# Kernel optimization log

Hardware: AMD Instinct MI355X
Metric: run time of the kernel (lower is better)

Reference implementation:

```python
import jax, jax.numpy as jnp
import numpy as np

B, N, C = 4, 8192, 512
H, Dh, G, R = 8, 64, 64, 2  # heads, dim_head, slice_num, mlp_ratio
EPS_LN = 1e-5
EPS_NORM = 1e-5


def _ln(x, g, b):
    m = jnp.mean(x, axis=-1, keepdims=True)
    v = jnp.var(x, axis=-1, keepdims=True)
    return (x - m) * jax.lax.rsqrt(v + EPS_LN) * g + b


def setup_inputs() -> dict:
    key = jax.random.key(0)
    ks = jax.random.split(key, 16)
    r = lambda k, shp: jax.random.normal(k, shp, jnp.float32) * 0.02
    inner = H * Dh
    return {
        "fx": jax.random.normal(ks[0], (B, N, C), jnp.float32),
        "ln1_g": jnp.ones((C,), jnp.float32), "ln1_b": jnp.zeros((C,), jnp.float32),
        "Wx": r(ks[1], (C, inner)), "bx": jnp.zeros((inner,), jnp.float32),
        "Wfx": r(ks[2], (C, inner)), "bfx": jnp.zeros((inner,), jnp.float32),
        "Wslice": r(ks[3], (Dh, G)), "bslice": jnp.zeros((G,), jnp.float32),
        "temperature": jnp.full((1, H, 1, 1), 0.5, jnp.float32),
        "Wq": r(ks[4], (Dh, Dh)), "Wk": r(ks[5], (Dh, Dh)), "Wv": r(ks[6], (Dh, Dh)),
        "Wout": r(ks[7], (inner, C)), "bout": jnp.zeros((C,), jnp.float32),
        "tln_g": jnp.ones((Dh,), jnp.float32), "tln_b": jnp.zeros((Dh,), jnp.float32),
        "Wm1": r(ks[8], (Dh, R * Dh)), "bm1": jnp.zeros((R * Dh,), jnp.float32),
        "Wm2": r(ks[9], (R * Dh, Dh)), "bm2": jnp.zeros((Dh,), jnp.float32),
    }


def reference(fx, ln1_g, ln1_b, Wx, bx, Wfx, bfx, Wslice, bslice, temperature,
              Wq, Wk, Wv, Wout, bout, tln_g, tln_b, Wm1, bm1, Wm2, bm2):
    fx_norm = _ln(fx, ln1_g, ln1_b)                          # [B,N,C]
    # _forward_slice: project to per-head mid features
    x_mid = (fx_norm @ Wx + bx).reshape(B, N, H, Dh).transpose(0, 2, 1, 3)   # [B,H,N,Dh]
    fx_mid = (fx_norm @ Wfx + bfx).reshape(B, N, H, Dh).transpose(0, 2, 1, 3)
    # _project_token: soft slice assignment + weighted pooling into G tokens
    logits = jnp.einsum('bhnd,dg->bhng', x_mid, Wslice) + bslice
    slice_w = jax.nn.softmax(logits / temperature, axis=-1)  # [B,H,N,G]
    slice_norm = jnp.sum(slice_w, axis=2)                    # [B,H,G]
    slice_tok = jnp.einsum('bhnd,bhng->bhgd', fx_mid, slice_w) / (slice_norm[..., None] + EPS_NORM)
    # attention over the small token set (G tokens)
    q = slice_tok @ Wq
    k = slice_tok @ Wk
    v = slice_tok @ Wv
    scale = Dh ** -0.5
    attn = jax.nn.softmax(jnp.einsum('bhgd,bhpd->bhgp', q, k) * scale, axis=-1)
    out_tok = jnp.einsum('bhgp,bhpd->bhgd', attn, v) + slice_tok
    # token MLP with residual
    h = _ln(out_tok, tln_g, tln_b)
    h = jax.nn.gelu(h @ Wm1 + bm1, approximate=False) @ Wm2 + bm2
    tokens = h + out_tok                                     # [B,H,G,Dh]
    # _deslice: weighted scatter back to N points, merge heads, out projection
    out_x = jnp.einsum('bhgd,bhng->bhnd', tokens, slice_w)
    out_x = out_x.transpose(0, 2, 1, 3).reshape(B, N, H * Dh)
    out = out_x @ Wout + bout
    return out + fx_norm
```

## Files before the change

kernel.cpp:

```cpp
#include <hip/hip_runtime.h>
#include <math.h>

#define B_ 4
#define N_ 8192
#define C_ 512
#define H_ 8
#define M_ (B_ * N_)

typedef __attribute__((ext_vector_type(8))) short bf16x8;
typedef __attribute__((ext_vector_type(4))) float f32x4;
typedef __attribute__((ext_vector_type(8))) unsigned short u16x8;
typedef __attribute__((ext_vector_type(4))) unsigned short u16x4;

__device__ __forceinline__ float b2f(unsigned short u) {
  union { unsigned int i; float f; } v;
  v.i = ((unsigned int)u) << 16;
  return v.f;
}
__device__ __forceinline__ unsigned short f2b(float f) {
  union { float f; unsigned int i; } v;
  v.f = f;
  unsigned int r = v.i + 0x7fff + ((v.i >> 16) & 1);
  return (unsigned short)(r >> 16);
}
__device__ __forceinline__ void gl_lds16(const void* g, void* l) {
  __builtin_amdgcn_global_load_lds(
      (const __attribute__((address_space(1))) unsigned int*)g,
      (__attribute__((address_space(3))) unsigned int*)l, 16, 0, 0);
}

__global__ __launch_bounds__(256) void ln_bf16(
    const float* __restrict__ x, const float* __restrict__ gam,
    const float* __restrict__ bet, unsigned short* __restrict__ y) {
  int wave = threadIdx.x >> 6, lane = threadIdx.x & 63;
  int row = (blockIdx.x << 2) + wave;
  const float4* xr = (const float4*)(x + (size_t)row * C_);
  float4 v0 = xr[lane], v1 = xr[lane + 64];
  float s = v0.x + v0.y + v0.z + v0.w + v1.x + v1.y + v1.z + v1.w;
  float q = v0.x * v0.x + v0.y * v0.y + v0.z * v0.z + v0.w * v0.w +
            v1.x * v1.x + v1.y * v1.y + v1.z * v1.z + v1.w * v1.w;
#pragma unroll
  for (int off = 32; off; off >>= 1) {
    s += __shfl_xor(s, off);
    q += __shfl_xor(q, off);
  }
  float mean = s * (1.0f / C_);
  float var = q * (1.0f / C_) - mean * mean;
  float rstd = rsqrtf(var + 1e-5f);
  const float4* gr = (const float4*)gam;
  const float4* br = (const float4*)bet;
  float4 g0 = gr[lane], g1 = gr[lane + 64];
  float4 b0 = br[lane], b1 = br[lane + 64];
  u16x4 oa, ob;
  oa.x = f2b((v0.x - mean) * rstd * g0.x + b0.x);
  oa.y = f2b((v0.y - mean) * rstd * g0.y + b0.y);
  oa.z = f2b((v0.z - mean) * rstd * g0.z + b0.z);
  oa.w = f2b((v0.w - mean) * rstd * g0.w + b0.w);
  ob.x = f2b((v1.x - mean) * rstd * g1.x + b1.x);
  ob.y = f2b((v1.y - mean) * rstd * g1.y + b1.y);
  ob.z = f2b((v1.z - mean) * rstd * g1.z + b1.z);
  ob.w = f2b((v1.w - mean) * rstd * g1.w + b1.w);
  unsigned short* yr = y + (size_t)row * C_;
  *(u16x4*)(yr + (lane << 2)) = oa;
  *(u16x4*)(yr + 256 + (lane << 2)) = ob;
}

__global__ __launch_bounds__(256) void prep_all(
    const float* __restrict__ Wx, const float* __restrict__ Wfx,
    const float* __restrict__ Wout, const float* __restrict__ Wsl,
    const float* __restrict__ Wq, const float* __restrict__ Wk,
    const float* __restrict__ Wv, const float* __restrict__ Wm1,
    const float* __restrict__ Wm2, unsigned short* __restrict__ WtX,
    unsigned short* __restrict__ WtF, unsigned short* __restrict__ WtO,
    unsigned short* __restrict__ wsf, unsigned short* __restrict__ wfr) {
  __shared__ float tile[64][65];
  int blk = blockIdx.x, t = threadIdx.x;
  if (blk < 192) {
    int which = blk >> 6, sub = blk & 63;
    const float* W = (which == 0) ? Wx : (which == 1) ? Wfx : Wout;
    unsigned short* Wt = (which == 0) ? WtX : (which == 1) ? WtF : WtO;
    int r0 = (sub >> 3) << 6, c0 = (sub & 7) << 6;
    int lr = t >> 4, lc = (t & 15) << 2;
#pragma unroll
    for (int p = 0; p < 4; p++) {
      float4 v = *(const float4*)(W + (size_t)(r0 + lr + p * 16) * 512 + c0 + lc);
      tile[lr + p * 16][lc + 0] = v.x;
      tile[lr + p * 16][lc + 1] = v.y;
      tile[lr + p * 16][lc + 2] = v.z;
      tile[lr + p * 16][lc + 3] = v.w;
    }
    __syncthreads();
    int on = t >> 2, ok = (t & 3) << 4;
    unsigned short tmp[16];
#pragma unroll
    for (int j = 0; j < 16; j++) tmp[j] = f2b(tile[ok + j][on]);
    unsigned short* op = Wt + (size_t)(c0 + on) * 512 + r0 + ok;
#pragma unroll
    for (int j4 = 0; j4 < 4; j4++)
      *(u16x4*)(op + (j4 << 2)) = *(u16x4*)(tmp + (j4 << 2));
  } else {
#pragma unroll
    for (int i = 0; i < 2; i++) {
      int idx = t + i * 256;
      int f = idx >> 6, l = idx & 63;
      int gt = f >> 1, ks = f & 1;
      int g = (gt << 4) + (l & 15);
      int d0 = (ks << 5) + ((l >> 4) << 3);
      unsigned short v[8];
#pragma unroll
      for (int jj = 0; jj < 8; jj++) v[jj] = f2b(Wsl[(size_t)(d0 + jj) * 64 + g]);
      *(u16x4*)(wsf + idx * 8) = *(u16x4*)v;
      *(u16x4*)(wsf + idx * 8 + 4) = *(u16x4*)(v + 4);
    }
    for (int task = t; task < 56 * 64; task += 256) {
      int fid = task >> 6, l = task & 63;
      const float* W;
      int stride, ct, ks;
      if (fid < 24) {
        W = (fid < 8) ? Wq : (fid < 16) ? Wk : Wv;
        int e = fid & 7;
        ct = e >> 1;
        ks = e & 1;
        stride = 64;
      } else if (fid < 40) {
        W = Wm1;
        int e = fid - 24;
        ct = e >> 1;
        ks = e & 1;
        stride = 128;
      } else {
        W = Wm2;
        int e = fid - 40;
        ct = e >> 2;
        ks = e & 3;
        stride = 64;
      }
      int d0 = (ks << 5) + ((l >> 4) << 3);
      int c = (ct << 4) + (l & 15);
      unsigned short v[8];
#pragma unroll
      for (int j = 0; j < 8; j++) v[j] = f2b(W[(size_t)(d0 + j) * stride + c]);
      *(u16x4*)(wfr + task * 8) = *(u16x4*)v;
      *(u16x4*)(wfr + task * 8 + 4) = *(u16x4*)(v + 4);
    }
  }
}

template <int DEC, bool BIASROW, bool OUTBF, bool RES>
__global__ __launch_bounds__(256) void gemm_bf16(
    const unsigned short* __restrict__ A, const unsigned short* __restrict__ Bt,
    const float* __restrict__ bias, const unsigned short* __restrict__ resid,
    void* __restrict__ Cout, size_t ldC) {
  __shared__ unsigned short lds[16384];
  const int t = threadIdx.x;
  const int w = t >> 6, l = t & 63;
  int bid = blockIdx.x;
  int xcd = bid & 7, q = bid >> 3;
  int bm, bn;
  if (DEC == 0) {
    bm = ((xcd << 5) + (q >> 2)) << 7;
    bn = (q & 3) << 7;
  } else {
    bn = ((xcd << 5) + (q >> 2)) << 7;
    bm = (q & 3) << 7;
  }
  const int wm = (w >> 1) << 6, wn = (w & 1) << 6;
  f32x4 acc[4][4];
#pragma unroll
  for (int mt = 0; mt < 4; mt++)
#pragma unroll
    for (int nt = 0; nt < 4; nt++) acc[mt][nt] = (f32x4){0.f, 0.f, 0.f, 0.f};

  const int srow = t >> 3;
  const int scol = (((t & 7) ^ ((t >> 3) & 7)) << 3);
  const unsigned short* gA = A + (size_t)(bm + srow) * 512 + scol;
  const unsigned short* gB = Bt + (size_t)(bn + srow) * 512 + scol;
  const int fr = l & 15, qq = l >> 4;

  for (int k0 = 0; k0 < 512; k0 += 64) {
#pragma unroll
    for (int i = 0; i < 4; i++)
      gl_lds16(gA + (size_t)(i << 5) * 512 + k0, lds + (i << 11) + (w << 9));
#pragma unroll
    for (int i = 0; i < 4; i++)
      gl_lds16(gB + (size_t)(i << 5) * 512 + k0, lds + 8192 + (i << 11) + (w << 9));
    __syncthreads();
#pragma unroll
    for (int kk = 0; kk < 2; kk++) {
      bf16x8 af[4], bfr[4];
#pragma unroll
      for (int mt = 0; mt < 4; mt++) {
        int row = wm + mt * 16 + fr;
        af[mt] = *(const bf16x8*)&lds[row * 64 + ((((kk << 2) + qq) ^ (fr & 7)) << 3)];
      }
#pragma unroll
      for (int nt = 0; nt < 4; nt++) {
        int row = wn + nt * 16 + fr;
        bfr[nt] = *(const bf16x8*)&lds[8192 + row * 64 + ((((kk << 2) + qq) ^ (fr & 7)) << 3)];
      }
#pragma unroll
      for (int mt = 0; mt < 4; mt++)
#pragma unroll
        for (int nt = 0; nt < 4; nt++)
          acc[mt][nt] = __builtin_amdgcn_mfma_f32_16x16x32_bf16(
              af[mt], bfr[nt], acc[mt][nt], 0, 0, 0);
    }
    __syncthreads();
  }

  const int col0 = bn + wn + (l & 15);
  const int row0 = bm + wm + ((l >> 4) << 2);
#pragma unroll
  for (int mt = 0; mt < 4; mt++) {
#pragma unroll
    for (int j = 0; j < 4; j++) {
      int row = row0 + mt * 16 + j;
#pragma unroll
      for (int nt = 0; nt < 4; nt++) {
        int col = col0 + nt * 16;
        float v = acc[mt][nt][j] + (BIASROW ? bias[row] : bias[col]);
        if (RES) v += b2f(resid[(size_t)row * ldC + col]);
        if (OUTBF)
          ((unsigned short*)Cout)[(size_t)row * ldC + col] = f2b(v);
        else
          ((float*)Cout)[(size_t)row * ldC + col] = v;
      }
    }
  }
}

__global__ __launch_bounds__(256) void pool_mfma(
    const unsigned short* __restrict__ xmid, const unsigned short* __restrict__ fxT,
    const unsigned short* __restrict__ wf, const float* __restrict__ bslice,
    const float* __restrict__ temp, float* __restrict__ tok_part,
    float* __restrict__ norm_part) {
  __shared__ unsigned short wT[4096];
  __shared__ float wred[4][64];
  int bid = blockIdx.x;
  int bh = bid >> 5, c = bid & 31;
  int b = bh >> 3, h = bh & 7;
  int t = threadIdx.x, w = t >> 6, l = t & 63;
  int n0 = c << 8;
  const int fr15 = l & 15, fs = l >> 4;

  bf16x8 wsf[4][2];
#pragma unroll
  for (int gt = 0; gt < 4; gt++)
#pragma unroll
    for (int ks = 0; ks < 2; ks++)
      wsf[gt][ks] = *(const bf16x8*)(wf + (((gt << 1) + ks) * 64 + l) * 8);
  float invt = 1.0f / temp[h];
  float bsl16[16];
#pragma unroll
  for (int gt = 0; gt < 4; gt++)
#pragma unroll
    for (int r = 0; r < 4; r++)
      bsl16[(gt << 2) + r] = bslice[(gt << 4) + (fs << 2) + r];

  f32x4 acc[4];
#pragma unroll
  for (int gt = 0; gt < 4; gt++) acc[gt] = (f32x4){0.f, 0.f, 0.f, 0.f};
  float nacc[16];
#pragma unroll
  for (int i = 0; i < 16; i++) nacc[i] = 0.f;

  const unsigned short* fxrow =
      fxT + (size_t)(h * 64 + w * 16 + fr15) * 32768 + b * N_ + n0 + (fs << 3);
  const int ncol = (w << 4) + fr15;

  for (int nn = 0; nn < 256; nn += 64) {
    size_t xrow = ((size_t)(b * N_ + n0 + nn + ncol) * 8 + h) << 6;
    bf16x8 xf0 = *(const bf16x8*)(xmid + xrow + (fs << 3));
    bf16x8 xf1 = *(const bf16x8*)(xmid + xrow + 32 + (fs << 3));
    f32x4 lg4[4];
#pragma unroll
    for (int gt = 0; gt < 4; gt++) {
      lg4[gt] = (f32x4){0.f, 0.f, 0.f, 0.f};
      lg4[gt] = __builtin_amdgcn_mfma_f32_16x16x32_bf16(wsf[gt][0], xf0, lg4[gt], 0, 0, 0);
      lg4[gt] = __builtin_amdgcn_mfma_f32_16x16x32_bf16(wsf[gt][1], xf1, lg4[gt], 0, 0, 0);
    }
    float p[16];
    float mx = -1e30f;
#pragma unroll
    for (int gt = 0; gt < 4; gt++)
#pragma unroll
      for (int r = 0; r < 4; r++) {
        float v = (lg4[gt][r] + bsl16[(gt << 2) + r]) * invt;
        p[(gt << 2) + r] = v;
        mx = fmaxf(mx, v);
      }
    mx = fmaxf(mx, __shfl_xor(mx, 16));
    mx = fmaxf(mx, __shfl_xor(mx, 32));
    float ssum = 0.f;
#pragma unroll
    for (int i = 0; i < 16; i++) {
      p[i] = __expf(p[i] - mx);
      ssum += p[i];
    }
    ssum += __shfl_xor(ssum, 16);
    ssum += __shfl_xor(ssum, 32);
    float inv = 1.0f / ssum;
#pragma unroll
    for (int i = 0; i < 16; i++) {
      p[i] *= inv;
      nacc[i] += p[i];
    }
    __syncthreads();
#pragma unroll
    for (int gt = 0; gt < 4; gt++)
#pragma unroll
      for (int r = 0; r < 4; r++) {
        int g = (gt << 4) + (fs << 2) + r;
        wT[(g << 6) + ((((ncol >> 3)) ^ (g & 7)) << 3) + (ncol & 7)] =
            f2b(p[(gt << 2) + r]);
      }
    __syncthreads();
#pragma unroll
    for (int kk = 0; kk < 2; kk++) {
      bf16x8 bfrag = *(const bf16x8*)(fxrow + nn + (kk << 5));
#pragma unroll
      for (int gt = 0; gt < 4; gt++) {
        int g = (gt << 4) + fr15;
        int slot = (kk << 2) + fs;
        bf16x8 af = *(const bf16x8*)&wT[(g << 6) + ((slot ^ (g & 7)) << 3)];
        acc[gt] = __builtin_amdgcn_mfma_f32_16x16x32_bf16(af, bfrag, acc[gt], 0, 0, 0);
      }
    }
  }
  float* op = tok_part + ((size_t)bid << 12);
#pragma unroll
  for (int gt = 0; gt < 4; gt++)
#pragma unroll
    for (int rr = 0; rr < 4; rr++)
      op[((gt << 4) + (fs << 2) + rr) * 64 + (w << 4) + fr15] = acc[gt][rr];
#pragma unroll
  for (int i = 0; i < 16; i++) {
    nacc[i] += __shfl_xor(nacc[i], 1);
    nacc[i] += __shfl_xor(nacc[i], 2);
    nacc[i] += __shfl_xor(nacc[i], 4);
    nacc[i] += __shfl_xor(nacc[i], 8);
  }
  if (fr15 == 0) {
#pragma unroll
    for (int i = 0; i < 16; i++)
      wred[w][((i >> 2) << 4) + (fs << 2) + (i & 3)] = nacc[i];
  }
  __syncthreads();
  if (t < 64)
    norm_part[((size_t)bid << 6) + t] =
        wred[0][t] + wred[1][t] + wred[2][t] + wred[3][t];
}

__device__ __forceinline__ float gelu_exact(float x) {
  return 0.5f * x * (1.0f + erff(x * 0.70710678118654752f));
}

__global__ __launch_bounds__(256) void token_mfma(
    const float* __restrict__ tok_part, const float* __restrict__ norm_part,
    const unsigned short* __restrict__ wfr, const float* __restrict__ tg,
    const float* __restrict__ tb, const float* __restrict__ bm1,
    const float* __restrict__ bm2, unsigned short* __restrict__ wtokf) {
  __shared__ __align__(16) char smem[54272];
  __shared__ float red[64];
  unsigned short* stb = (unsigned short*)smem;
  float* st32 = (float*)(smem + 9216);
  unsigned short* hmld = (unsigned short*)(smem + 9216);
  unsigned short* qld = (unsigned short*)(smem + 26624);
  unsigned short* kld = (unsigned short*)(smem + 35840);
  unsigned short* vtl = (unsigned short*)(smem + 45056);

  int bh = blockIdx.x, t = threadIdx.x, w = t >> 6, l = t & 63;
  const int fr = l & 15, fq = l >> 4;

  if (t < 64) {
    float s = 0.f;
    const float* np = norm_part + ((size_t)bh << 11);
#pragma unroll
    for (int cc = 0; cc < 32; cc++) s += np[(cc << 6) + t];
    red[t] = s;
  }
  {
    float a16[16];
#pragma unroll
    for (int j = 0; j < 16; j++) a16[j] = 0.f;
    const float* tp = tok_part + ((size_t)bh << 17) + (t << 4);
    for (int cc = 0; cc < 32; cc++) {
      const float* pp = tp + (cc << 12);
#pragma unroll
      for (int j4 = 0; j4 < 4; j4++) {
        float4 v = *(const float4*)(pp + (j4 << 2));
        a16[j4 * 4 + 0] += v.x;
        a16[j4 * 4 + 1] += v.y;
        a16[j4 * 4 + 2] += v.z;
        a16[j4 * 4 + 3] += v.w;
      }
    }
    __syncthreads();
    float rn = 1.0f / (red[t >> 2] + 1e-5f);
    int r = t >> 2, c0 = (t & 3) << 4;
    unsigned short tv[16];
#pragma unroll
    for (int j = 0; j < 16; j++) {
      float v = a16[j] * rn;
      st32[r * 68 + c0 + j] = v;
      tv[j] = f2b(v);
    }
    *(u16x8*)&stb[r * 72 + c0] = *(u16x8*)tv;
    *(u16x8*)&stb[r * 72 + c0 + 8] = *(u16x8*)(tv + 8);
  }
  __syncthreads();

  const int orow = (w << 4) + (fq << 2);

  {
    bf16x8 af[2];
#pragma unroll
    for (int ks = 0; ks < 2; ks++)
      af[ks] = *(const bf16x8*)&stb[((w << 4) + fr) * 72 + (ks << 5) + (fq << 3)];
    f32x4 aq[4], ak[4], av[4];
#pragma unroll
    for (int ct = 0; ct < 4; ct++) {
      aq[ct] = (f32x4){0.f, 0.f, 0.f, 0.f};
      ak[ct] = (f32x4){0.f, 0.f, 0.f, 0.f};
      av[ct] = (f32x4){0.f, 0.f, 0.f, 0.f};
    }
#pragma unroll
    for (int ct = 0; ct < 4; ct++)
#pragma unroll
      for (int ks = 0; ks < 2; ks++) {
        bf16x8 bq = *(const bf16x8*)&wfr[(((ct << 1) + ks) * 64 + l) * 8];
        aq[ct] = __builtin_amdgcn_mfma_f32_16x16x32_bf16(af[ks], bq, aq[ct], 0, 0, 0);
      }
#pragma unroll
    for (int ct = 0; ct < 4; ct++)
#pragma unroll
      for (int ks = 0; ks < 2; ks++) {
        bf16x8 bk = *(const bf16x8*)&wfr[((8 + (ct << 1) + ks) * 64 + l) * 8];
        ak[ct] = __builtin_amdgcn_mfma_f32_16x16x32_bf16(af[ks], bk, ak[ct], 0, 0, 0);
      }
#pragma unroll
    for (int ct = 0; ct < 4; ct++)
#pragma unroll
      for (int ks = 0; ks < 2; ks++) {
        bf16x8 bv = *(const bf16x8*)&wfr[((16 + (ct << 1) + ks) * 64 + l) * 8];
        av[ct] = __builtin_amdgcn_mfma_f32_16x16x32_bf16(af[ks], bv, av[ct], 0, 0, 0);
      }
#pragma unroll
    for (int ct = 0; ct < 4; ct++) {
#pragma unroll
      for (int rr = 0; rr < 4; rr++) {
        qld[(orow + rr) * 72 + (ct << 4) + fr] = f2b(aq[ct][rr]);
        kld[(orow + rr) * 72 + (ct << 4) + fr] = f2b(ak[ct][rr]);
      }
      u16x4 vp;
      vp.x = f2b(av[ct][0]);
      vp.y = f2b(av[ct][1]);
      vp.z = f2b(av[ct][2]);
      vp.w = f2b(av[ct][3]);
      *(u16x4*)&vtl[((ct << 4) + fr) * 72 + orow] = vp;
    }
  }
  __syncthreads();

  {
    bf16x8 aq[2];
#pragma unroll
    for (int ks = 0; ks < 2; ks++)
      aq[ks] = *(const bf16x8*)&qld[((w << 4) + fr) * 72 + (ks << 5) + (fq << 3)];
    f32x4 accs[4];
#pragma unroll
    for (int nt = 0; nt < 4; nt++) accs[nt] = (f32x4){0.f, 0.f, 0.f, 0.f};
#pragma unroll
    for (int nt = 0; nt < 4; nt++)
#pragma unroll
      for (int ks = 0; ks < 2; ks++) {
        bf16x8 bk = *(const bf16x8*)&kld[((nt << 4) + fr) * 72 + (ks << 5) + (fq << 3)];
        accs[nt] = __builtin_amdgcn_mfma_f32_16x16x32_bf16(aq[ks], bk, accs[nt], 0, 0, 0);
      }
#pragma unroll
    for (int rr = 0; rr < 4; rr++) {
      float v0 = accs[0][rr] * 0.125f, v1 = accs[1][rr] * 0.125f;
      float v2 = accs[2][rr] * 0.125f, v3 = accs[3][rr] * 0.125f;
      float mx = fmaxf(fmaxf(v0, v1), fmaxf(v2, v3));
      mx = fmaxf(mx, __shfl_xor(mx, 1));
      mx = fmaxf(mx, __shfl_xor(mx, 2));
      mx = fmaxf(mx, __shfl_xor(mx, 4));
      mx = fmaxf(mx, __shfl_xor(mx, 8));
      float e0 = __expf(v0 - mx), e1 = __expf(v1 - mx);
      float e2 = __expf(v2 - mx), e3 = __expf(v3 - mx);
      float ss = e0 + e1 + e2 + e3;
      ss += __shfl_xor(ss, 1);
      ss += __shfl_xor(ss, 2);
      ss += __shfl_xor(ss, 4);
      ss += __shfl_xor(ss, 8);
      float inv = 1.0f / ss;
      stb[(orow + rr) * 72 + 0 * 16 + fr] = f2b(e0 * inv);
      stb[(orow + rr) * 72 + 1 * 16 + fr] = f2b(e1 * inv);
      stb[(orow + rr) * 72 + 2 * 16 + fr] = f2b(e2 * inv);
      stb[(orow + rr) * 72 + 3 * 16 + fr] = f2b(e3 * inv);
    }
  }
  __syncthreads();

  float o16[4][4];
  {
    bf16x8 ap[2];
#pragma unroll
    for (int ks = 0; ks < 2; ks++)
      ap[ks] = *(const bf16x8*)&stb[((w << 4) + fr) * 72 + (ks << 5) + (fq << 3)];
    f32x4 acco[4];
#pragma unroll
    for (int ct = 0; ct < 4; ct++) acco[ct] = (f32x4){0.f, 0.f, 0.f, 0.f};
#pragma unroll
    for (int ct = 0; ct < 4; ct++)
#pragma unroll
      for (int ks = 0; ks < 2; ks++) {
        bf16x8 bv = *(const bf16x8*)&vtl[((ct << 4) + fr) * 72 + (ks << 5) + (fq << 3)];
        acco[ct] = __builtin_amdgcn_mfma_f32_16x16x32_bf16(ap[ks], bv, acco[ct], 0, 0, 0);
      }
    float tgv[4], tbv[4];
#pragma unroll
    for (int ct = 0; ct < 4; ct++) {
      tgv[ct] = tg[(ct << 4) + fr];
      tbv[ct] = tb[(ct << 4) + fr];
    }
#pragma unroll
    for (int ct = 0; ct < 4; ct++)
#pragma unroll
      for (int rr = 0; rr < 4; rr++)
        o16[ct][rr] = acco[ct][rr] + st32[(orow + rr) * 68 + (ct << 4) + fr];
#pragma unroll
    for (int rr = 0; rr < 4; rr++) {
      float sm = o16[0][rr] + o16[1][rr] + o16[2][rr] + o16[3][rr];
      float sq = o16[0][rr] * o16[0][rr] + o16[1][rr] * o16[1][rr] +
                 o16[2][rr] * o16[2][rr] + o16[3][rr] * o16[3][rr];
      sm += __shfl_xor(sm, 1);
      sm += __shfl_xor(sm, 2);
      sm += __shfl_xor(sm, 4);
      sm += __shfl_xor(sm, 8);
      sq += __shfl_xor(sq, 1);
      sq += __shfl_xor(sq, 2);
      sq += __shfl_xor(sq, 4);
      sq += __shfl_xor(sq, 8);
      float mean = sm * (1.0f / 64.0f);
      float var = sq * (1.0f / 64.0f) - mean * mean;
      float rstd = rsqrtf(var + 1e-5f);
#pragma unroll
      for (int ct = 0; ct < 4; ct++) {
        float hv = (o16[ct][rr] - mean) * rstd * tgv[ct] + tbv[ct];
        qld[(orow + rr) * 72 + (ct << 4) + fr] = f2b(hv);
      }
    }
  }
  __syncthreads();

  {
    bf16x8 ah[2];
#pragma unroll
    for (int ks = 0; ks < 2; ks++)
      ah[ks] = *(const bf16x8*)&qld[((w << 4) + fr) * 72 + (ks << 5) + (fq << 3)];
    f32x4 accm[8];
#pragma unroll
    for (int et = 0; et < 8; et++) accm[et] = (f32x4){0.f, 0.f, 0.f, 0.f};
#pragma unroll
    for (int et = 0; et < 8; et++)
#pragma unroll
      for (int ks = 0; ks < 2; ks++) {
        bf16x8 bm = *(const bf16x8*)&wfr[((24 + (et << 1) + ks) * 64 + l) * 8];
        accm[et] = __builtin_amdgcn_mfma_f32_16x16x32_bf16(ah[ks], bm, accm[et], 0, 0, 0);
      }
#pragma unroll
    for (int et = 0; et < 8; et++) {
      float bv = bm1[(et << 4) + fr];
#pragma unroll
      for (int rr = 0; rr < 4; rr++) {
        float x = accm[et][rr] + bv;
        hmld[(orow + rr) * 136 + (et << 4) + fr] = f2b(gelu_exact(x));
      }
    }
  }
  __syncthreads();

  {
    bf16x8 ahm[4];
#pragma unroll
    for (int ks = 0; ks < 4; ks++)
      ahm[ks] = *(const bf16x8*)&hmld[((w << 4) + fr) * 136 + (ks << 5) + (fq << 3)];
    f32x4 acc2[4];
#pragma unroll
    for (int ct = 0; ct < 4; ct++) acc2[ct] = (f32x4){0.f, 0.f, 0.f, 0.f};
#pragma unroll
    for (int ct = 0; ct < 4; ct++)
#pragma unroll
      for (int ks = 0; ks < 4; ks++) {
        bf16x8 bw = *(const bf16x8*)&wfr[((40 + (ct << 2) + ks) * 64 + l) * 8];
        acc2[ct] = __builtin_amdgcn_mfma_f32_16x16x32_bf16(ahm[ks], bw, acc2[ct], 0, 0, 0);
      }
#pragma unroll
    for (int ct = 0; ct < 4; ct++) {
      float bv = bm2[(ct << 4) + fr];
#pragma unroll
      for (int rr = 0; rr < 4; rr++)
        stb[(orow + rr) * 72 + (ct << 4) + fr] =
            f2b(acc2[ct][rr] + bv + o16[ct][rr]);
    }
  }
  __syncthreads();
  {
#pragma unroll
    for (int e = 0; e < 2; e++) {
      int fid = (w << 1) + e;
      int d = (w << 4) + (l & 15);
      int g0 = (e << 5) + ((l >> 4) << 3);
      unsigned short v[8];
#pragma unroll
      for (int j = 0; j < 8; j++) v[j] = stb[(g0 + j) * 72 + d];
      unsigned short* op = wtokf + (((size_t)bh << 3) + fid) * 512 + (l << 3);
      *(u16x4*)op = *(u16x4*)v;
      *(u16x4*)(op + 4) = *(u16x4*)(v + 4);
    }
  }
}

__global__ __launch_bounds__(256) void deslice_mfma(
    const unsigned short* __restrict__ wtokf, const unsigned short* __restrict__ xmid,
    const unsigned short* __restrict__ wf, const float* __restrict__ bslice,
    const float* __restrict__ temp, unsigned short* __restrict__ outx) {
  __shared__ unsigned short pex[4][1024];
  int bid = blockIdx.x;
  int bh = bid >> 5, c = bid & 31;
  int b = bh >> 3, h = bh & 7;
  int t = threadIdx.x, w = t >> 6, l = t & 63;
  const int fr = l & 15, fq = l >> 4;
  unsigned short* pw = pex[w];

  bf16x8 ta[4][2];
  const unsigned short* fp = wtokf + ((size_t)bh << 12);
#pragma unroll
  for (int mt = 0; mt < 4; mt++)
#pragma unroll
    for (int ks = 0; ks < 2; ks++)
      ta[mt][ks] = *(const bf16x8*)(fp + (((mt << 1) + ks) << 9) + (l << 3));
  bf16x8 wsf[4][2];
#pragma unroll
  for (int gt = 0; gt < 4; gt++)
#pragma unroll
    for (int ks = 0; ks < 2; ks++)
      wsf[gt][ks] = *(const bf16x8*)(wf + (((gt << 1) + ks) * 64 + l) * 8);
  float invt = 1.0f / temp[h];
  float bsl16[16];
#pragma unroll
  for (int gt = 0; gt < 4; gt++)
#pragma unroll
    for (int r = 0; r < 4; r++)
      bsl16[(gt << 2) + r] = bslice[(gt << 4) + (fq << 2) + r];

  int n0 = (c << 8) + (w << 6);
#pragma unroll
  for (int ntile = 0; ntile < 4; ntile++) {
    int nb = n0 + (ntile << 4);
    size_t rowb = ((size_t)(b * N_ + nb + fr) * 8 + h) << 6;
    bf16x8 xf0 = *(const bf16x8*)(xmid + rowb + (fq << 3));
    bf16x8 xf1 = *(const bf16x8*)(xmid + rowb + 32 + (fq << 3));
    f32x4 lg4[4];
#pragma unroll
    for (int gt = 0; gt < 4; gt++) {
      lg4[gt] = (f32x4){0.f, 0.f, 0.f, 0.f};
      lg4[gt] = __builtin_amdgcn_mfma_f32_16x16x32_bf16(wsf[gt][0], xf0, lg4[gt], 0, 0, 0);
      lg4[gt] = __builtin_amdgcn_mfma_f32_16x16x32_bf16(wsf[gt][1], xf1, lg4[gt], 0, 0, 0);
    }
    float p[16];
    float mx = -1e30f;
#pragma unroll
    for (int gt = 0; gt < 4; gt++)
#pragma unroll
      for (int r = 0; r < 4; r++) {
        float v = (lg4[gt][r] + bsl16[(gt << 2) + r]) * invt;
        p[(gt << 2) + r] = v;
        mx = fmaxf(mx, v);
      }
    mx = fmaxf(mx, __shfl_xor(mx, 16));
    mx = fmaxf(mx, __shfl_xor(mx, 32));
    float ssum = 0.f;
#pragma unroll
    for (int i = 0; i < 16; i++) {
      p[i] = __expf(p[i] - mx);
      ssum += p[i];
    }
    ssum += __shfl_xor(ssum, 16);
    ssum += __shfl_xor(ssum, 32);
    float inv = 1.0f / ssum;
#pragma unroll
    for (int gt = 0; gt < 4; gt++)
#pragma unroll
      for (int r = 0; r < 4; r++) {
        int g = (gt << 4) + (fq << 2) + r;
        pw[(fr << 6) + (((g >> 3) ^ (fr & 7)) << 3) + (g & 7)] =
            f2b(p[(gt << 2) + r] * inv);
      }
    bf16x8 b0 = *(const bf16x8*)&pw[(fr << 6) + ((fq ^ (fr & 7)) << 3)];
    bf16x8 b1 = *(const bf16x8*)&pw[(fr << 6) + (((4 + fq) ^ (fr & 7)) << 3)];
    f32x4 acc[4];
#pragma unroll
    for (int mt = 0; mt < 4; mt++) acc[mt] = (f32x4){0.f, 0.f, 0.f, 0.f};
#pragma unroll
    for (int mt = 0; mt < 4; mt++) {
      acc[mt] = __builtin_amdgcn_mfma_f32_16x16x32_bf16(ta[mt][0], b0, acc[mt], 0, 0, 0);
      acc[mt] = __builtin_amdgcn_mfma_f32_16x16x32_bf16(ta[mt][1], b1, acc[mt], 0, 0, 0);
    }
    unsigned short* op = outx + rowb + (fq << 2);
#pragma unroll
    for (int mt = 0; mt < 4; mt++) {
      u16x4 pk;
      pk.x = f2b(acc[mt][0]);
      pk.y = f2b(acc[mt][1]);
      pk.z = f2b(acc[mt][2]);
      pk.w = f2b(acc[mt][3]);
      *(u16x4*)(op + (mt << 4)) = pk;
    }
  }
}

extern "C" void kernel_launch(void* const* d_in, const int* in_sizes, int n_in,
                              void* d_out, int out_size, void* d_ws,
                              size_t ws_size, hipStream_t stream) {
  const float* fx = (const float*)d_in[0];
  const float* ln1g = (const float*)d_in[1];
  const float* ln1b = (const float*)d_in[2];
  const float* Wx = (const float*)d_in[3];
  const float* bx = (const float*)d_in[4];
  const float* Wfx = (const float*)d_in[5];
  const float* bfx = (const float*)d_in[6];
  const float* Wsl = (const float*)d_in[7];
  const float* bsl = (const float*)d_in[8];
  const float* temp = (const float*)d_in[9];
  const float* Wq = (const float*)d_in[10];
  const float* Wk = (const float*)d_in[11];
  const float* Wv = (const float*)d_in[12];
  const float* Wout = (const float*)d_in[13];
  const float* bout = (const float*)d_in[14];
  const float* tlng = (const float*)d_in[15];
  const float* tlnb = (const float*)d_in[16];
  const float* Wm1 = (const float*)d_in[17];
  const float* bm1 = (const float*)d_in[18];
  const float* Wm2 = (const float*)d_in[19];
  const float* bm2 = (const float*)d_in[20];
  float* out = (float*)d_out;

  char* p = (char*)d_ws;
  const size_t MC2 = (size_t)M_ * 512 * 2;
  unsigned short* fxn = (unsigned short*)p;  p += MC2;
  unsigned short* buf1 = (unsigned short*)p; p += MC2;
  unsigned short* bufT = (unsigned short*)p; p += MC2;
  unsigned short* WtX = (unsigned short*)p;  p += 512 * 512 * 2;
  unsigned short* WtF = (unsigned short*)p;  p += 512 * 512 * 2;
  unsigned short* WtO = (unsigned short*)p;  p += 512 * 512 * 2;
  unsigned short* wsf = (unsigned short*)p;  p += 8192;
  unsigned short* wfr = (unsigned short*)p;  p += 56 * 512 * 2;
  unsigned short* wtokf = (unsigned short*)p; p += (size_t)32 * 8 * 512 * 2;
  float* tok_part = (float*)p;  p += (size_t)1024 * 4096 * 4;
  float* norm_part = (float*)p; p += (size_t)1024 * 64 * 4;

  ln_bf16<<<M_ / 4, 256, 0, stream>>>(fx, ln1g, ln1b, fxn);
  prep_all<<<193, 256, 0, stream>>>(Wx, Wfx, Wout, Wsl, Wq, Wk, Wv, Wm1, Wm2,
                                    WtX, WtF, WtO, wsf, wfr);
  gemm_bf16<0, false, true, false><<<1024, 256, 0, stream>>>(fxn, WtX, bx, nullptr, buf1, 512);
  gemm_bf16<1, true, true, false><<<1024, 256, 0, stream>>>(WtF, fxn, bfx, nullptr, bufT, 32768);
  pool_mfma<<<1024, 256, 0, stream>>>(buf1, bufT, wsf, bsl, temp, tok_part, norm_part);
  token_mfma<<<32, 256, 0, stream>>>(tok_part, norm_part, wfr, tlng, tlnb, bm1, bm2, wtokf);
  deslice_mfma<<<1024, 256, 0, stream>>>(wtokf, buf1, wsf, bsl, temp, bufT);
  gemm_bf16<0, false, false, true><<<1024, 256, 0, stream>>>(bufT, WtO, bout, fxn, out, 512);
}
```

Baseline: 169.3 us.

## Fuse x and fx projection GEMMs into one dual-output kernel with LDS transpose

Replaces the two separate projection GEMMs (Wx and Wfx) with one kernel that loads each A tile once and runs MFMAs against both weight tiles into two accumulator sets. The second output is transposed through LDS before being stored, replacing the old swapped-operand GEMM that produced the transposed layout. This removes one full read of the normalized activations and one kernel launch. In exchange it doubles the accumulator registers, which may lower occupancy, and raises LDS use to 48KB per block.

```diff
diff --git a/kernel.cpp b/kernel.cpp
--- a/kernel.cpp
+++ b/kernel.cpp
@@ -146,24 +146,135 @@
   }
 }
 
-template <int DEC, bool BIASROW, bool OUTBF, bool RES>
-__global__ __launch_bounds__(256) void gemm_bf16(
+__global__ __launch_bounds__(256) void gemm_dual(
+    const unsigned short* __restrict__ A, const unsigned short* __restrict__ B1t,
+    const unsigned short* __restrict__ B2t, const float* __restrict__ bias1,
+    const float* __restrict__ bias2, unsigned short* __restrict__ out1,
+    unsigned short* __restrict__ outT) {
+  __shared__ unsigned short lds[24576];
+  const int t = threadIdx.x;
+  const int w = t >> 6, l = t & 63;
+  int bid = blockIdx.x;
+  int xcd = bid & 7, q = bid >> 3;
+  const int bm = ((xcd << 5) + (q >> 2)) << 7;
+  const int bn = (q & 3) << 7;
+  const int wm = (w >> 1) << 6, wn = (w & 1) << 6;
+  f32x4 acc1[4][4], acc2[4][4];
+#pragma unroll
+  for (int mt = 0; mt < 4; mt++)
+#pragma unroll
+    for (int nt = 0; nt < 4; nt++) {
+      acc1[mt][nt] = (f32x4){0.f, 0.f, 0.f, 0.f};
+      acc2[mt][nt] = (f32x4){0.f, 0.f, 0.f, 0.f};
+    }
+
+  const int srow = t >> 3;
+  const int scol = (((t & 7) ^ ((t >> 3) & 7)) << 3);
+  const unsigned short* gA = A + (size_t)(bm + srow) * 512 + scol;
+  const unsigned short* gB1 = B1t + (size_t)(bn + srow) * 512 + scol;
+  const unsigned short* gB2 = B2t + (size_t)(bn + srow) * 512 + scol;
+  const int fr = l & 15, fq = l >> 4;
+
+  for (int k0 = 0; k0 < 512; k0 += 64) {
+#pragma unroll
+    for (int i = 0; i < 4; i++)
+      gl_lds16(gA + (size_t)(i << 5) * 512 + k0, lds + (i << 11) + (w << 9));
+#pragma unroll
+    for (int i = 0; i < 4; i++)
+      gl_lds16(gB1 + (size_t)(i << 5) * 512 + k0, lds + 8192 + (i << 11) + (w << 9));
+#pragma unroll
+    for (int i = 0; i < 4; i++)
+      gl_lds16(gB2 + (size_t)(i << 5) * 512 + k0, lds + 16384 + (i << 11) + (w << 9));
+    __syncthreads();
+#pragma unroll
+    for (int kk = 0; kk < 2; kk++) {
+      const int ps = ((((kk << 2) + fq) ^ (fr & 7)) << 3);
+      bf16x8 af[4];
+#pragma unroll
+      for (int mt = 0; mt < 4; mt++)
+        af[mt] = *(const bf16x8*)&lds[(wm + mt * 16 + fr) * 64 + ps];
+      {
+        bf16x8 b1[4];
+#pragma unroll
+        for (int nt = 0; nt < 4; nt++)
+          b1[nt] = *(const bf16x8*)&lds[8192 + (wn + nt * 16 + fr) * 64 + ps];
+#pragma unroll
+        for (int mt = 0; mt < 4; mt++)
+#pragma unroll
+          for (int nt = 0; nt < 4; nt++)
+            acc1[mt][nt] = __builtin_amdgcn_mfma_f32_16x16x32_bf16(
+                af[mt], b1[nt], acc1[mt][nt], 0, 0, 0);
+      }
+      {
+        bf16x8 b2[4];
+#pragma unroll
+        for (int nt = 0; nt < 4; nt++)
+          b2[nt] = *(const bf16x8*)&lds[16384 + (wn + nt * 16 + fr) * 64 + ps];
+#pragma unroll
+        for (int mt = 0; mt < 4; mt++)
+#pragma unroll
+          for (int nt = 0; nt < 4; nt++)
+            acc2[mt][nt] = __builtin_amdgcn_mfma_f32_16x16x32_bf16(
+                af[mt], b2[nt], acc2[mt][nt], 0, 0, 0);
+      }
+    }
+    __syncthreads();
+  }
+
+  const int col0 = bn + wn + fr;
+  const int row0 = bm + wm + (fq << 2);
+#pragma unroll
+  for (int mt = 0; mt < 4; mt++)
+#pragma unroll
+    for (int j = 0; j < 4; j++) {
+      int row = row0 + mt * 16 + j;
+#pragma unroll
+      for (int nt = 0; nt < 4; nt++) {
+        int col = col0 + nt * 16;
+        out1[(size_t)row * 512 + col] = f2b(acc1[mt][nt][j] + bias1[col]);
+      }
+    }
+
+  unsigned short* T = lds + (w << 12);
+#pragma unroll
+  for (int nt = 0; nt < 4; nt++) {
+    int f_loc = (nt << 4) + fr;
+    float bv = bias2[bn + wn + f_loc];
+#pragma unroll
+    for (int mt = 0; mt < 4; mt++) {
+      u16x4 pk;
+      pk.x = f2b(acc2[mt][nt][0] + bv);
+      pk.y = f2b(acc2[mt][nt][1] + bv);
+      pk.z = f2b(acc2[mt][nt][2] + bv);
+      pk.w = f2b(acc2[mt][nt][3] + bv);
+      int slot = (mt << 1) + (fq >> 1);
+      int off = ((slot ^ (f_loc & 7)) << 3) + ((fq & 1) << 2);
+      *(u16x4*)&T[f_loc * 64 + off] = pk;
+    }
+  }
+  asm volatile("s_waitcnt lgkmcnt(0)" ::: "memory");
+  __builtin_amdgcn_sched_barrier(0);
+#pragma unroll
+  for (int s = 0; s < 8; s++) {
+    int f_loc = (s << 3) + (l >> 3);
+    int m0 = (l & 7) << 3;
+    int phys = (l & 7) ^ (f_loc & 7);
+    u16x8 v = *(const u16x8*)&T[f_loc * 64 + (phys << 3)];
+    *(u16x8*)(outT + (size_t)(bn + wn + f_loc) * 32768 + bm + wm + m0) = v;
+  }
+}
+
+__global__ __launch_bounds__(256) void gemm_out(
     const unsigned short* __restrict__ A, const unsigned short* __restrict__ Bt,
     const float* __restrict__ bias, const unsigned short* __restrict__ resid,
-    void* __restrict__ Cout, size_t ldC) {
+    float* __restrict__ Cout) {
   __shared__ unsigned short lds[16384];
   const int t = threadIdx.x;
   const int w = t >> 6, l = t & 63;
   int bid = blockIdx.x;
   int xcd = bid & 7, q = bid >> 3;
-  int bm, bn;
-  if (DEC == 0) {
-    bm = ((xcd << 5) + (q >> 2)) << 7;
-    bn = (q & 3) << 7;
-  } else {
-    bn = ((xcd << 5) + (q >> 2)) << 7;
-    bm = (q & 3) << 7;
-  }
+  const int bm = ((xcd << 5) + (q >> 2)) << 7;
+  const int bn = (q & 3) << 7;
   const int wm = (w >> 1) << 6, wn = (w & 1) << 6;
   f32x4 acc[4][4];
 #pragma unroll
@@ -218,12 +329,8 @@
 #pragma unroll
       for (int nt = 0; nt < 4; nt++) {
         int col = col0 + nt * 16;
-        float v = acc[mt][nt][j] + (BIASROW ? bias[row] : bias[col]);
-        if (RES) v += b2f(resid[(size_t)row * ldC + col]);
-        if (OUTBF)
-          ((unsigned short*)Cout)[(size_t)row * ldC + col] = f2b(v);
-        else
-          ((float*)Cout)[(size_t)row * ldC + col] = v;
+        float v = acc[mt][nt][j] + bias[col] + b2f(resid[(size_t)row * 512 + col]);
+        Cout[(size_t)row * 512 + col] = v;
       }
     }
   }
@@ -764,10 +871,9 @@
   ln_bf16<<<M_ / 4, 256, 0, stream>>>(fx, ln1g, ln1b, fxn);
   prep_all<<<193, 256, 0, stream>>>(Wx, Wfx, Wout, Wsl, Wq, Wk, Wv, Wm1, Wm2,
                                     WtX, WtF, WtO, wsf, wfr);
-  gemm_bf16<0, false, true, false><<<1024, 256, 0, stream>>>(fxn, WtX, bx, nullptr, buf1, 512);
-  gemm_bf16<1, true, true, false><<<1024, 256, 0, stream>>>(WtF, fxn, bfx, nullptr, bufT, 32768);
+  gemm_dual<<<1024, 256, 0, stream>>>(fxn, WtX, WtF, bx, bfx, buf1, bufT);
   pool_mfma<<<1024, 256, 0, stream>>>(buf1, bufT, wsf, bsl, temp, tok_part, norm_part);
   token_mfma<<<32, 256, 0, stream>>>(tok_part, norm_part, wfr, tlng, tlnb, bm1, bm2, wtokf);
   deslice_mfma<<<1024, 256, 0, stream>>>(wtokf, buf1, wsf, bsl, temp, bufT);
-  gemm_bf16<0, false, false, true><<<1024, 256, 0, stream>>>(bufT, WtO, bout, fxn, out, 512);
-}
+  gemm_out<<<1024, 256, 0, stream>>>(bufT, WtO, bout, fxn, out);
+}
```

Result: slower. 182.5 us (+7.8%).
